# Performance work log

Hardware: AMD Instinct MI355X
Metric: run time of the kernel (lower is better)

The kernel has to match this reference:

```python
import jax, jax.numpy as jnp
import numpy as np

N_NODES = 300000
DIM = 64
NNZ = 4800000


def setup_inputs() -> dict:
    key = jax.random.key(0)
    ks = jax.random.split(key, 8)
    emb_all = 0.1 * jax.random.normal(ks[0], (N_NODES, DIM), dtype=jnp.float32)
    # edge values ~ symmetric-normalized adjacency scale (avg degree 16 -> ~1/16)
    vals = jax.random.uniform(ks[1], (NNZ,), dtype=jnp.float32) * (1.0 / 16.0)
    vals2 = jax.random.uniform(ks[2], (NNZ,), dtype=jnp.float32) * (1.0 / 16.0)
    rows = jnp.sort(jax.random.randint(ks[3], (NNZ,), 0, N_NODES, dtype=jnp.int32))
    cols = jax.random.randint(ks[4], (NNZ,), 0, N_NODES, dtype=jnp.int32)
    rows2 = jnp.sort(jax.random.randint(ks[5], (NNZ,), 0, N_NODES, dtype=jnp.int32))
    cols2 = jax.random.randint(ks[6], (NNZ,), 0, N_NODES, dtype=jnp.int32)
    return {
        "emb_all": emb_all,
        "vals": vals,
        "vals2": vals2,
        "rows": rows,
        "cols": cols,
        "rows2": rows2,
        "cols2": cols2,
        "n_layers": 3,
        "num_users": 100000,
    }


def _spmm(rows, cols, vals, x, n):
    # sparse [n,n] @ dense [n,d] via gather + segment-sum
    return jax.ops.segment_sum(vals[:, None] * x[cols], rows, num_segments=n)


def _pearson(x, y):
    # per-row pearson correlation over the last (latent) dim -> [N]
    xd = x - jnp.mean(x, axis=-1, keepdims=True)
    yd = y - jnp.mean(y, axis=-1, keepdims=True)
    num = jnp.sum(xd * yd, axis=-1)
    den = jnp.sqrt(jnp.sum(xd * xd, axis=-1)) * jnp.sqrt(jnp.sum(yd * yd, axis=-1))
    den = jnp.where(den < 1e-7, jnp.float32(1e-7), den)
    return num / den


def reference(emb_all, vals, vals2, rows, cols, rows2, cols2, n_layers, num_users):
    n = emb_all.shape[0]
    e0 = emb_all
    embs2 = [e0]
    # layer 0: plain LightGCN propagation on G
    e = _spmm(rows, cols, vals, e0, n)
    embs2.append(e)
    # layers 1..n_layers: pearson-gated propagation on G2
    for _ in range(n_layers):
        b = _pearson(embs2[-1], e0)  # [N]
        prop = _spmm(rows2, cols2, vals2, embs2[-1], n)
        e = b[:, None] * prop + (1.0 - b)[:, None] * e0
        embs2.append(e)
    light_out = jnp.mean(jnp.stack(embs2, axis=1), axis=1)  # [N, d]
    users = light_out[:num_users]
    items = light_out[num_users:]
    return users, items
```

## Files before the change

### kernel.cpp

```cpp
#include <hip/hip_runtime.h>

#define DIM 64

typedef __attribute__((ext_vector_type(4))) float f4;
typedef __attribute__((ext_vector_type(2))) float f2;
typedef __attribute__((ext_vector_type(4))) unsigned int u4;
typedef __attribute__((ext_vector_type(2))) unsigned int u2;

#define SEL_LO 0x01000504u
#define SEL_HI 0x03020706u
#define ONE2   0x3f803f80u

__device__ __forceinline__ float bflo(unsigned u) { return __uint_as_float(u << 16); }
__device__ __forceinline__ float bfhi(unsigned u) { return __uint_as_float(u & 0xffff0000u); }
__device__ __forceinline__ unsigned bfr(float f) {
    unsigned u = __float_as_uint(f);
    return (u + 0x7fffu + ((u >> 16) & 1u)) >> 16;
}
__device__ __forceinline__ unsigned packbf(float e, float o) { return bfr(e) | (bfr(o) << 16); }
__device__ __forceinline__ unsigned cvtpk(float lo, float hi) {
    unsigned r;
    asm("v_cvt_pk_bf16_f32 %0, %1, %2" : "=v"(r) : "v"(lo), "v"(hi));
    return r;
}
__device__ __forceinline__ float dot2bf(unsigned a, unsigned b, float c) {
    float d;
    asm("v_dot2_f32_bf16 %0, %1, %2, %3" : "=v"(d) : "v"(a), "v"(b), "v"(c));
    return d;
}
__device__ __forceinline__ float gsum8(float v) {
    v += __shfl_xor(v, 1, 64);
    v += __shfl_xor(v, 2, 64);
    v += __shfl_xor(v, 4, 64);
    return v;
}

__global__ void build_row_ptr2_kernel(const int* __restrict__ rowsA, int nnzA,
                                      const int* __restrict__ rowsB, int nnzB,
                                      int n, int* __restrict__ rpA,
                                      int* __restrict__ rpB) {
    int i = blockIdx.x * blockDim.x + threadIdx.x;
    const int* rows; int nnz; int* rp; int r;
    if (i <= n) { rows = rowsA; nnz = nnzA; rp = rpA; r = i; }
    else {
        r = i - (n + 1);
        if (r > n) return;
        rows = rowsB; nnz = nnzB; rp = rpB;
    }
    int lo = 0, hi = nnz;
    while (lo < hi) {
        int mid = (lo + hi) >> 1;
        if (rows[mid] < r) lo = mid + 1; else hi = mid;
    }
    rp[r] = lo;
}

__global__ void cvt_bf16_kernel(const float* __restrict__ in,
                                unsigned int* __restrict__ out, int n8) {
    int i = blockIdx.x * blockDim.x + threadIdx.x;
    if (i >= n8) return;
    const f4* p = (const f4*)in + 2 * (size_t)i;
    f4 a = p[0], b = p[1];
    u4 o;
    o.x = packbf(a.x, a.y); o.y = packbf(a.z, a.w);
    o.z = packbf(b.x, b.y); o.w = packbf(b.z, b.w);
    ((u4*)out)[i] = o;
}

template <int MODE>
__global__ __launch_bounds__(256) void layer_kernel(
    const unsigned short* __restrict__ t0,
    const unsigned short* __restrict__ eprev,
    const float* __restrict__ vals, const int* __restrict__ cols,
    const int* __restrict__ rp, int n,
    unsigned short* __restrict__ enew,
    const unsigned short* __restrict__ e1t,
    const unsigned short* __restrict__ e2t,
    f2* __restrict__ stats, float* __restrict__ bbuf,
    float* __restrict__ out)
{
    const int tid  = threadIdx.x;
    const int lane = tid & 63;
    const int j    = lane & 7;
    const int wave = blockIdx.x * (blockDim.x >> 6) + (tid >> 6);
    const int rowg = wave * 8 + (lane >> 3);
    const bool valid = rowg < n;
    const int rg   = valid ? rowg : n - 1;

    const int start = rp[rg];
    const int end   = rp[rg + 1];
    const int len   = valid ? (end - start) : 0;
    const int b0    = start & ~1;
    const int doff  = b0 - start;

    int ml = len;
    ml = max(ml, __shfl_xor(ml, 8, 64));
    ml = max(ml, __shfl_xor(ml, 16, 64));
    ml = max(ml, __shfl_xor(ml, 32, 64));
    const int steps = (ml + 8) >> 3;

    const char* tb8 = (const char*)eprev;
    const unsigned joff = (unsigned)(j << 4);
    const size_t ro = (size_t)rg << 6;

    float bcoef = 0.f;
    if (MODE != 0) bcoef = bbuf[rg];
    u4 yr = *((const u4*)(t0 + ro) + j);
    f2 st = {};
    if (MODE == 1) st = stats[rg];

    float acc[8] = {0.f, 0.f, 0.f, 0.f, 0.f, 0.f, 0.f, 0.f};

    for (int s = 0; s < steps; ++s) {
        const int k = b0 + (s << 3);
        u2 c01 = __builtin_nontemporal_load((const u2*)(cols + k));
        u2 c23 = __builtin_nontemporal_load((const u2*)(cols + k + 2));
        u2 c45 = __builtin_nontemporal_load((const u2*)(cols + k + 4));
        u2 c67 = __builtin_nontemporal_load((const u2*)(cols + k + 6));
        f2 v01 = __builtin_nontemporal_load((const f2*)(vals + k));
        f2 v23 = __builtin_nontemporal_load((const f2*)(vals + k + 2));
        f2 v45 = __builtin_nontemporal_load((const f2*)(vals + k + 4));
        f2 v67 = __builtin_nontemporal_load((const f2*)(vals + k + 6));
        const int rel = (s << 3) + doff;
        bool ok0 = (unsigned)(rel)     < (unsigned)len;
        bool ok1 = (unsigned)(rel + 1) < (unsigned)len;
        bool ok2 = (unsigned)(rel + 2) < (unsigned)len;
        bool ok3 = (unsigned)(rel + 3) < (unsigned)len;
        bool ok4 = (unsigned)(rel + 4) < (unsigned)len;
        bool ok5 = (unsigned)(rel + 5) < (unsigned)len;
        bool ok6 = (unsigned)(rel + 6) < (unsigned)len;
        bool ok7 = (unsigned)(rel + 7) < (unsigned)len;
        unsigned cc0 = ok0 ? (unsigned)c01.x : 0u;
        unsigned cc1 = ok1 ? (unsigned)c01.y : 0u;
        unsigned cc2 = ok2 ? (unsigned)c23.x : 0u;
        unsigned cc3 = ok3 ? (unsigned)c23.y : 0u;
        unsigned cc4 = ok4 ? (unsigned)c45.x : 0u;
        unsigned cc5 = ok5 ? (unsigned)c45.y : 0u;
        unsigned cc6 = ok6 ? (unsigned)c67.x : 0u;
        unsigned cc7 = ok7 ? (unsigned)c67.y : 0u;
        u4 g0 = *(const u4*)(tb8 + ((cc0 << 7) + joff));
        u4 g1 = *(const u4*)(tb8 + ((cc1 << 7) + joff));
        u4 g2 = *(const u4*)(tb8 + ((cc2 << 7) + joff));
        u4 g3 = *(const u4*)(tb8 + ((cc3 << 7) + joff));
        u4 g4 = *(const u4*)(tb8 + ((cc4 << 7) + joff));
        u4 g5 = *(const u4*)(tb8 + ((cc5 << 7) + joff));
        u4 g6 = *(const u4*)(tb8 + ((cc6 << 7) + joff));
        u4 g7 = *(const u4*)(tb8 + ((cc7 << 7) + joff));
        float w0 = ok0 ? v01.x : 0.f;
        float w1 = ok1 ? v01.y : 0.f;
        float w2 = ok2 ? v23.x : 0.f;
        float w3 = ok3 ? v23.y : 0.f;
        float w4 = ok4 ? v45.x : 0.f;
        float w5 = ok5 ? v45.y : 0.f;
        float w6 = ok6 ? v67.x : 0.f;
        float w7 = ok7 ? v67.y : 0.f;
        unsigned vp01 = cvtpk(w0, w1);
        unsigned vp23 = cvtpk(w2, w3);
        unsigned vp45 = cvtpk(w4, w5);
        unsigned vp67 = cvtpk(w6, w7);
#define CONSUME(ga, gb, vp)                                                    \
        acc[0] = dot2bf(__builtin_amdgcn_perm(ga.x, gb.x, SEL_LO), vp, acc[0]);\
        acc[1] = dot2bf(__builtin_amdgcn_perm(ga.x, gb.x, SEL_HI), vp, acc[1]);\
        acc[2] = dot2bf(__builtin_amdgcn_perm(ga.y, gb.y, SEL_LO), vp, acc[2]);\
        acc[3] = dot2bf(__builtin_amdgcn_perm(ga.y, gb.y, SEL_HI), vp, acc[3]);\
        acc[4] = dot2bf(__builtin_amdgcn_perm(ga.z, gb.z, SEL_LO), vp, acc[4]);\
        acc[5] = dot2bf(__builtin_amdgcn_perm(ga.z, gb.z, SEL_HI), vp, acc[5]);\
        acc[6] = dot2bf(__builtin_amdgcn_perm(ga.w, gb.w, SEL_LO), vp, acc[6]);\
        acc[7] = dot2bf(__builtin_amdgcn_perm(ga.w, gb.w, SEL_HI), vp, acc[7]);
        CONSUME(g0, g1, vp01)
        CONSUME(g2, g3, vp23)
        CONSUME(g4, g5, vp45)
        CONSUME(g6, g7, vp67)
#undef CONSUME
    }

    if (MODE == 0) {
        float sy  = dot2bf(yr.x, ONE2,
                    dot2bf(yr.y, ONE2, dot2bf(yr.z, ONE2, dot2bf(yr.w, ONE2, 0.f))));
        float syy = dot2bf(yr.x, yr.x,
                    dot2bf(yr.y, yr.y, dot2bf(yr.z, yr.z, dot2bf(yr.w, yr.w, 0.f))));
        sy = gsum8(sy); syy = gsum8(syy);
        float my  = sy * (1.f / 64.f);
        float vy  = syy - sy * my;
        float svy = sqrtf(fmaxf(vy, 0.f));
        u4 o;
        o.x = cvtpk(acc[0], acc[1]); o.y = cvtpk(acc[2], acc[3]);
        o.z = cvtpk(acc[4], acc[5]); o.w = cvtpk(acc[6], acc[7]);
        float sx  = dot2bf(o.x, ONE2,
                    dot2bf(o.y, ONE2, dot2bf(o.z, ONE2, dot2bf(o.w, ONE2, 0.f))));
        float sxx = dot2bf(o.x, o.x,
                    dot2bf(o.y, o.y, dot2bf(o.z, o.z, dot2bf(o.w, o.w, 0.f))));
        float sxy = dot2bf(o.x, yr.x,
                    dot2bf(o.y, yr.y, dot2bf(o.z, yr.z, dot2bf(o.w, yr.w, 0.f))));
        sx = gsum8(sx); sxx = gsum8(sxx); sxy = gsum8(sxy);
        float mx  = sx * (1.f / 64.f);
        float num = sxy - sx * my;
        float vx  = sxx - sx * mx;
        float den = sqrtf(fmaxf(vx, 0.f)) * svy;
        den = fmaxf(den, 1e-7f);
        float bn = num / den;
        if (valid) {
            if (j == 0) {
                f2 s2; s2.x = my; s2.y = svy;
                __builtin_nontemporal_store(s2, stats + rg);
                __builtin_nontemporal_store(bn, bbuf + rg);
            }
            __builtin_nontemporal_store(o, (u4*)(enew + ro) + j);
        }
        return;
    }

    const float ob = 1.f - bcoef;

    if (MODE == 1) {
        float y0[8] = { bflo(yr.x), bfhi(yr.x), bflo(yr.y), bfhi(yr.y),
                        bflo(yr.z), bfhi(yr.z), bflo(yr.w), bfhi(yr.w) };
        u4 o;
        o.x = cvtpk(bcoef * acc[0] + ob * y0[0], bcoef * acc[1] + ob * y0[1]);
        o.y = cvtpk(bcoef * acc[2] + ob * y0[2], bcoef * acc[3] + ob * y0[3]);
        o.z = cvtpk(bcoef * acc[4] + ob * y0[4], bcoef * acc[5] + ob * y0[5]);
        o.w = cvtpk(bcoef * acc[6] + ob * y0[6], bcoef * acc[7] + ob * y0[7]);
        float sx  = dot2bf(o.x, ONE2,
                    dot2bf(o.y, ONE2, dot2bf(o.z, ONE2, dot2bf(o.w, ONE2, 0.f))));
        float sxx = dot2bf(o.x, o.x,
                    dot2bf(o.y, o.y, dot2bf(o.z, o.z, dot2bf(o.w, o.w, 0.f))));
        float sxy = dot2bf(o.x, yr.x,
                    dot2bf(o.y, yr.y, dot2bf(o.z, yr.z, dot2bf(o.w, yr.w, 0.f))));
        sx = gsum8(sx); sxx = gsum8(sxx); sxy = gsum8(sxy);
        float mx  = sx * (1.f / 64.f);
        float num = sxy - sx * st.x;
        float vx  = sxx - sx * mx;
        float den = sqrtf(fmaxf(vx, 0.f)) * st.y;
        den = fmaxf(den, 1e-7f);
        float bn = num / den;
        if (valid) {
            if (j == 0) __builtin_nontemporal_store(bn, bbuf + rg);
            __builtin_nontemporal_store(o, (u4*)(enew + ro) + j);
        }
    } else {
        float y0[8] = { bflo(yr.x), bfhi(yr.x), bflo(yr.y), bfhi(yr.y),
                        bflo(yr.z), bfhi(yr.z), bflo(yr.w), bfhi(yr.w) };
        u4 xr = *((const u4*)(eprev + ro) + j);
        float xp[8] = { bflo(xr.x), bfhi(xr.x), bflo(xr.y), bfhi(xr.y),
                        bflo(xr.z), bfhi(xr.z), bflo(xr.w), bfhi(xr.w) };
        u4 r1 = *((const u4*)(e1t + ro) + j);
        u4 r2 = *((const u4*)(e2t + ro) + j);
        float s[8];
        s[0] = y0[0] + bflo(r1.x) + bflo(r2.x) + xp[0] + (bcoef * acc[0] + ob * y0[0]);
        s[1] = y0[1] + bfhi(r1.x) + bfhi(r2.x) + xp[1] + (bcoef * acc[1] + ob * y0[1]);
        s[2] = y0[2] + bflo(r1.y) + bflo(r2.y) + xp[2] + (bcoef * acc[2] + ob * y0[2]);
        s[3] = y0[3] + bfhi(r1.y) + bfhi(r2.y) + xp[3] + (bcoef * acc[3] + ob * y0[3]);
        s[4] = y0[4] + bflo(r1.z) + bflo(r2.z) + xp[4] + (bcoef * acc[4] + ob * y0[4]);
        s[5] = y0[5] + bfhi(r1.z) + bfhi(r2.z) + xp[5] + (bcoef * acc[5] + ob * y0[5]);
        s[6] = y0[6] + bflo(r1.w) + bflo(r2.w) + xp[6] + (bcoef * acc[6] + ob * y0[6]);
        s[7] = y0[7] + bfhi(r1.w) + bfhi(r2.w) + xp[7] + (bcoef * acc[7] + ob * y0[7]);
        if (valid) {
            f4 o0 = { s[0] * 0.2f, s[1] * 0.2f, s[2] * 0.2f, s[3] * 0.2f };
            f4 o1 = { s[4] * 0.2f, s[5] * 0.2f, s[6] * 0.2f, s[7] * 0.2f };
            f4* op = (f4*)(out + ro) + 2 * j;
            __builtin_nontemporal_store(o0, op);
            __builtin_nontemporal_store(o1, op + 1);
        }
    }
}

extern "C" void kernel_launch(void* const* d_in, const int* in_sizes, int n_in,
                              void* d_out, int out_size, void* d_ws, size_t ws_size,
                              hipStream_t stream) {
    const float* emb   = (const float*)d_in[0];
    const float* vals  = (const float*)d_in[1];
    const float* vals2 = (const float*)d_in[2];
    const int*   rows  = (const int*)d_in[3];
    const int*   cols  = (const int*)d_in[4];
    const int*   rows2 = (const int*)d_in[5];
    const int*   cols2 = (const int*)d_in[6];

    const int n    = in_sizes[0] / DIM;
    const int nnz  = in_sizes[1];
    const int nnz2 = in_sizes[2];

    float* out = (float*)d_out;

    char*  ws       = (char*)d_ws;
    size_t rp_bytes = (((size_t)(n + 1) * sizeof(int)) + 255) & ~(size_t)255;
    size_t st_bytes = (((size_t)n * sizeof(f2)) + 255) & ~(size_t)255;
    size_t bb_bytes = (((size_t)n * sizeof(float)) + 255) & ~(size_t)255;
    size_t tb_bytes = (size_t)n * DIM * sizeof(unsigned short);
    int*   rp1 = (int*)ws;
    int*   rp2 = (int*)(ws + rp_bytes);
    f2*    ST  = (f2*)(ws + 2 * rp_bytes);
    float* BB  = (float*)(ws + 2 * rp_bytes + st_bytes);
    unsigned short* T0 = (unsigned short*)(ws + 2 * rp_bytes + st_bytes + bb_bytes);
    unsigned short* E1 = (unsigned short*)((char*)T0 + tb_bytes);
    unsigned short* E2 = (unsigned short*)((char*)E1 + tb_bytes);
    unsigned short* E3 = (unsigned short*)((char*)E2 + tb_bytes);

    const int tb = 256;
    build_row_ptr2_kernel<<<(2 * (n + 1) + tb - 1) / tb, tb, 0, stream>>>(
        rows, nnz, rows2, nnz2, n, rp1, rp2);

    const int n8 = n * DIM / 8;
    cvt_bf16_kernel<<<(n8 + tb - 1) / tb, tb, 0, stream>>>(emb, (unsigned int*)T0, n8);

    const int waves = (n + 7) / 8;
    const int grid  = (waves + 3) / 4;
    layer_kernel<0><<<grid, tb, 0, stream>>>(T0, T0, vals, cols, rp1, n,
                                             E1, T0, T0, ST, BB, out);
    layer_kernel<1><<<grid, tb, 0, stream>>>(T0, E1, vals2, cols2, rp2, n,
                                             E2, T0, T0, ST, BB, out);
    layer_kernel<1><<<grid, tb, 0, stream>>>(T0, E2, vals2, cols2, rp2, n,
                                             E3, T0, T0, ST, BB, out);
    layer_kernel<2><<<grid, tb, 0, stream>>>(T0, E3, vals2, cols2, rp2, n,
                                             E3, E1, E2, ST, BB, out);
}
```

Baseline: 503.9 us.

## Gather neighbor embeddings from scaled FP8 tables instead of BF16

Each layer now writes a scaled FP8 copy of its embeddings alongside the BF16 copy, and the SpMM gather reads 8 bytes per lane from the FP8 table instead of 16. Accumulation moves to packed FP32 multiply-adds after FP8-to-FP32 unpacking. Layer 1 also pre-sums e1 and e2 into one buffer, so the final layer reads fewer tensors. This roughly halves the random gather traffic that dominates SpMM, at the cost of FP8 precision loss in the propagated values and extra stores per layer.

```diff
diff --git a/kernel.cpp b/kernel.cpp
--- a/kernel.cpp
+++ b/kernel.cpp
@@ -1,15 +1,15 @@
 #include <hip/hip_runtime.h>
 
 #define DIM 64
+#define SC  32.0f
+#define ISC 0.03125f
 
 typedef __attribute__((ext_vector_type(4))) float f4;
 typedef __attribute__((ext_vector_type(2))) float f2;
 typedef __attribute__((ext_vector_type(4))) unsigned int u4;
 typedef __attribute__((ext_vector_type(2))) unsigned int u2;
 
-#define SEL_LO 0x01000504u
-#define SEL_HI 0x03020706u
-#define ONE2   0x3f803f80u
+#define ONE2 0x3f803f80u
 
 __device__ __forceinline__ float bflo(unsigned u) { return __uint_as_float(u << 16); }
 __device__ __forceinline__ float bfhi(unsigned u) { return __uint_as_float(u & 0xffff0000u); }
@@ -55,8 +55,9 @@
     rp[r] = lo;
 }
 
-__global__ void cvt_bf16_kernel(const float* __restrict__ in,
-                                unsigned int* __restrict__ out, int n8) {
+__global__ void cvt_kernel(const float* __restrict__ in,
+                           unsigned int* __restrict__ obf,
+                           unsigned char* __restrict__ of8, int n8) {
     int i = blockIdx.x * blockDim.x + threadIdx.x;
     if (i >= n8) return;
     const f4* p = (const f4*)in + 2 * (size_t)i;
@@ -64,18 +65,27 @@
     u4 o;
     o.x = packbf(a.x, a.y); o.y = packbf(a.z, a.w);
     o.z = packbf(b.x, b.y); o.w = packbf(b.z, b.w);
-    ((u4*)out)[i] = o;
-}
-
-template <int MODE>
+    ((u4*)obf)[i] = o;
+    int lo = 0, hi = 0;
+    lo = __builtin_amdgcn_cvt_pk_fp8_f32(a.x * SC, a.y * SC, lo, false);
+    lo = __builtin_amdgcn_cvt_pk_fp8_f32(a.z * SC, a.w * SC, lo, true);
+    hi = __builtin_amdgcn_cvt_pk_fp8_f32(b.x * SC, b.y * SC, hi, false);
+    hi = __builtin_amdgcn_cvt_pk_fp8_f32(b.z * SC, b.w * SC, hi, true);
+    u2 w8; w8.x = (unsigned)lo; w8.y = (unsigned)hi;
+    ((u2*)of8)[i] = w8;
+}
+
+template <int MODE, bool SUM>
 __global__ __launch_bounds__(256) void layer_kernel(
     const unsigned short* __restrict__ t0,
-    const unsigned short* __restrict__ eprev,
+    const unsigned char*  __restrict__ gtab,
     const float* __restrict__ vals, const int* __restrict__ cols,
     const int* __restrict__ rp, int n,
-    unsigned short* __restrict__ enew,
-    const unsigned short* __restrict__ e1t,
-    const unsigned short* __restrict__ e2t,
+    unsigned short* __restrict__ bfout,
+    unsigned char*  __restrict__ f8out,
+    const unsigned short* __restrict__ e1in,
+    const unsigned short* __restrict__ e3in,
+    const unsigned short* __restrict__ s12in,
     f2* __restrict__ stats, float* __restrict__ bbuf,
     float* __restrict__ out)
 {
@@ -99,17 +109,16 @@
     ml = max(ml, __shfl_xor(ml, 32, 64));
     const int steps = (ml + 8) >> 3;
 
-    const char* tb8 = (const char*)eprev;
-    const unsigned joff = (unsigned)(j << 4);
+    const unsigned joff8 = (unsigned)(j << 3);
     const size_t ro = (size_t)rg << 6;
 
     float bcoef = 0.f;
-    if (MODE != 0) bcoef = bbuf[rg];
-    u4 yr = *((const u4*)(t0 + ro) + j);
+    if (MODE != 0) bcoef = __builtin_nontemporal_load(bbuf + rg);
+    u4 yr = __builtin_nontemporal_load((const u4*)(t0 + ro) + j);
     f2 st = {};
-    if (MODE == 1) st = stats[rg];
-
-    float acc[8] = {0.f, 0.f, 0.f, 0.f, 0.f, 0.f, 0.f, 0.f};
+    if (MODE == 1) st = __builtin_nontemporal_load(stats + rg);
+
+    f2 a01 = {0.f, 0.f}, a23 = {0.f, 0.f}, a45 = {0.f, 0.f}, a67 = {0.f, 0.f};
 
     for (int s = 0; s < steps; ++s) {
         const int k = b0 + (s << 3);
@@ -138,14 +147,14 @@
         unsigned cc5 = ok5 ? (unsigned)c45.y : 0u;
         unsigned cc6 = ok6 ? (unsigned)c67.x : 0u;
         unsigned cc7 = ok7 ? (unsigned)c67.y : 0u;
-        u4 g0 = *(const u4*)(tb8 + ((cc0 << 7) + joff));
-        u4 g1 = *(const u4*)(tb8 + ((cc1 << 7) + joff));
-        u4 g2 = *(const u4*)(tb8 + ((cc2 << 7) + joff));
-        u4 g3 = *(const u4*)(tb8 + ((cc3 << 7) + joff));
-        u4 g4 = *(const u4*)(tb8 + ((cc4 << 7) + joff));
-        u4 g5 = *(const u4*)(tb8 + ((cc5 << 7) + joff));
-        u4 g6 = *(const u4*)(tb8 + ((cc6 << 7) + joff));
-        u4 g7 = *(const u4*)(tb8 + ((cc7 << 7) + joff));
+        u2 g0 = *(const u2*)(gtab + ((cc0 << 6) + joff8));
+        u2 g1 = *(const u2*)(gtab + ((cc1 << 6) + joff8));
+        u2 g2 = *(const u2*)(gtab + ((cc2 << 6) + joff8));
+        u2 g3 = *(const u2*)(gtab + ((cc3 << 6) + joff8));
+        u2 g4 = *(const u2*)(gtab + ((cc4 << 6) + joff8));
+        u2 g5 = *(const u2*)(gtab + ((cc5 << 6) + joff8));
+        u2 g6 = *(const u2*)(gtab + ((cc6 << 6) + joff8));
+        u2 g7 = *(const u2*)(gtab + ((cc7 << 6) + joff8));
         float w0 = ok0 ? v01.x : 0.f;
         float w1 = ok1 ? v01.y : 0.f;
         float w2 = ok2 ? v23.x : 0.f;
@@ -154,25 +163,21 @@
         float w5 = ok5 ? v45.y : 0.f;
         float w6 = ok6 ? v67.x : 0.f;
         float w7 = ok7 ? v67.y : 0.f;
-        unsigned vp01 = cvtpk(w0, w1);
-        unsigned vp23 = cvtpk(w2, w3);
-        unsigned vp45 = cvtpk(w4, w5);
-        unsigned vp67 = cvtpk(w6, w7);
-#define CONSUME(ga, gb, vp)                                                    \
-        acc[0] = dot2bf(__builtin_amdgcn_perm(ga.x, gb.x, SEL_LO), vp, acc[0]);\
-        acc[1] = dot2bf(__builtin_amdgcn_perm(ga.x, gb.x, SEL_HI), vp, acc[1]);\
-        acc[2] = dot2bf(__builtin_amdgcn_perm(ga.y, gb.y, SEL_LO), vp, acc[2]);\
-        acc[3] = dot2bf(__builtin_amdgcn_perm(ga.y, gb.y, SEL_HI), vp, acc[3]);\
-        acc[4] = dot2bf(__builtin_amdgcn_perm(ga.z, gb.z, SEL_LO), vp, acc[4]);\
-        acc[5] = dot2bf(__builtin_amdgcn_perm(ga.z, gb.z, SEL_HI), vp, acc[5]);\
-        acc[6] = dot2bf(__builtin_amdgcn_perm(ga.w, gb.w, SEL_LO), vp, acc[6]);\
-        acc[7] = dot2bf(__builtin_amdgcn_perm(ga.w, gb.w, SEL_HI), vp, acc[7]);
-        CONSUME(g0, g1, vp01)
-        CONSUME(g2, g3, vp23)
-        CONSUME(g4, g5, vp45)
-        CONSUME(g6, g7, vp67)
-#undef CONSUME
-    }
+#define CONS(gg, ww) {                                                        \
+        f2 wv; wv.x = (ww); wv.y = (ww);                                      \
+        f2 p0 = __builtin_amdgcn_cvt_pk_f32_fp8((int)gg.x, false);            \
+        f2 p1 = __builtin_amdgcn_cvt_pk_f32_fp8((int)gg.x, true);             \
+        f2 p2 = __builtin_amdgcn_cvt_pk_f32_fp8((int)gg.y, false);            \
+        f2 p3 = __builtin_amdgcn_cvt_pk_f32_fp8((int)gg.y, true);             \
+        a01 += wv * p0; a23 += wv * p1; a45 += wv * p2; a67 += wv * p3;       \
+    }
+        CONS(g0, w0) CONS(g1, w1) CONS(g2, w2) CONS(g3, w3)
+        CONS(g4, w4) CONS(g5, w5) CONS(g6, w6) CONS(g7, w7)
+#undef CONS
+    }
+
+    float acc[8] = { a01.x * ISC, a01.y * ISC, a23.x * ISC, a23.y * ISC,
+                     a45.x * ISC, a45.y * ISC, a67.x * ISC, a67.y * ISC };
 
     if (MODE == 0) {
         float sy  = dot2bf(yr.x, ONE2,
@@ -205,21 +210,29 @@
                 __builtin_nontemporal_store(s2, stats + rg);
                 __builtin_nontemporal_store(bn, bbuf + rg);
             }
-            __builtin_nontemporal_store(o, (u4*)(enew + ro) + j);
+            __builtin_nontemporal_store(o, (u4*)(bfout + ro) + j);
+            int lo = 0, hi = 0;
+            lo = __builtin_amdgcn_cvt_pk_fp8_f32(acc[0] * SC, acc[1] * SC, lo, false);
+            lo = __builtin_amdgcn_cvt_pk_fp8_f32(acc[2] * SC, acc[3] * SC, lo, true);
+            hi = __builtin_amdgcn_cvt_pk_fp8_f32(acc[4] * SC, acc[5] * SC, hi, false);
+            hi = __builtin_amdgcn_cvt_pk_fp8_f32(acc[6] * SC, acc[7] * SC, hi, true);
+            u2 w8; w8.x = (unsigned)lo; w8.y = (unsigned)hi;
+            __builtin_nontemporal_store(w8, (u2*)(f8out + (ro  )) + j);
         }
         return;
     }
 
     const float ob = 1.f - bcoef;
+    float y0[8] = { bflo(yr.x), bfhi(yr.x), bflo(yr.y), bfhi(yr.y),
+                    bflo(yr.z), bfhi(yr.z), bflo(yr.w), bfhi(yr.w) };
+    float en[8];
+    #pragma unroll
+    for (int i = 0; i < 8; ++i) en[i] = bcoef * acc[i] + ob * y0[i];
 
     if (MODE == 1) {
-        float y0[8] = { bflo(yr.x), bfhi(yr.x), bflo(yr.y), bfhi(yr.y),
-                        bflo(yr.z), bfhi(yr.z), bflo(yr.w), bfhi(yr.w) };
         u4 o;
-        o.x = cvtpk(bcoef * acc[0] + ob * y0[0], bcoef * acc[1] + ob * y0[1]);
-        o.y = cvtpk(bcoef * acc[2] + ob * y0[2], bcoef * acc[3] + ob * y0[3]);
-        o.z = cvtpk(bcoef * acc[4] + ob * y0[4], bcoef * acc[5] + ob * y0[5]);
-        o.w = cvtpk(bcoef * acc[6] + ob * y0[6], bcoef * acc[7] + ob * y0[7]);
+        o.x = cvtpk(en[0], en[1]); o.y = cvtpk(en[2], en[3]);
+        o.z = cvtpk(en[4], en[5]); o.w = cvtpk(en[6], en[7]);
         float sx  = dot2bf(o.x, ONE2,
                     dot2bf(o.y, ONE2, dot2bf(o.z, ONE2, dot2bf(o.w, ONE2, 0.f))));
         float sxx = dot2bf(o.x, o.x,
@@ -235,25 +248,37 @@
         float bn = num / den;
         if (valid) {
             if (j == 0) __builtin_nontemporal_store(bn, bbuf + rg);
-            __builtin_nontemporal_store(o, (u4*)(enew + ro) + j);
+            if (SUM) {
+                u4 e1r = __builtin_nontemporal_load((const u4*)(e1in + ro) + j);
+                u4 so;
+                so.x = packbf(bflo(e1r.x) + en[0], bfhi(e1r.x) + en[1]);
+                so.y = packbf(bflo(e1r.y) + en[2], bfhi(e1r.y) + en[3]);
+                so.z = packbf(bflo(e1r.z) + en[4], bfhi(e1r.z) + en[5]);
+                so.w = packbf(bflo(e1r.w) + en[6], bfhi(e1r.w) + en[7]);
+                __builtin_nontemporal_store(so, (u4*)(bfout + ro) + j);
+            } else {
+                __builtin_nontemporal_store(o, (u4*)(bfout + ro) + j);
+            }
+            int lo = 0, hi = 0;
+            lo = __builtin_amdgcn_cvt_pk_fp8_f32(en[0] * SC, en[1] * SC, lo, false);
+            lo = __builtin_amdgcn_cvt_pk_fp8_f32(en[2] * SC, en[3] * SC, lo, true);
+            hi = __builtin_amdgcn_cvt_pk_fp8_f32(en[4] * SC, en[5] * SC, hi, false);
+            hi = __builtin_amdgcn_cvt_pk_fp8_f32(en[6] * SC, en[7] * SC, hi, true);
+            u2 w8; w8.x = (unsigned)lo; w8.y = (unsigned)hi;
+            __builtin_nontemporal_store(w8, (u2*)(f8out + ro) + j);
         }
     } else {
-        float y0[8] = { bflo(yr.x), bfhi(yr.x), bflo(yr.y), bfhi(yr.y),
-                        bflo(yr.z), bfhi(yr.z), bflo(yr.w), bfhi(yr.w) };
-        u4 xr = *((const u4*)(eprev + ro) + j);
-        float xp[8] = { bflo(xr.x), bfhi(xr.x), bflo(xr.y), bfhi(xr.y),
-                        bflo(xr.z), bfhi(xr.z), bflo(xr.w), bfhi(xr.w) };
-        u4 r1 = *((const u4*)(e1t + ro) + j);
-        u4 r2 = *((const u4*)(e2t + ro) + j);
+        u4 xr  = __builtin_nontemporal_load((const u4*)(e3in + ro) + j);
+        u4 s12 = __builtin_nontemporal_load((const u4*)(s12in + ro) + j);
         float s[8];
-        s[0] = y0[0] + bflo(r1.x) + bflo(r2.x) + xp[0] + (bcoef * acc[0] + ob * y0[0]);
-        s[1] = y0[1] + bfhi(r1.x) + bfhi(r2.x) + xp[1] + (bcoef * acc[1] + ob * y0[1]);
-        s[2] = y0[2] + bflo(r1.y) + bflo(r2.y) + xp[2] + (bcoef * acc[2] + ob * y0[2]);
-        s[3] = y0[3] + bfhi(r1.y) + bfhi(r2.y) + xp[3] + (bcoef * acc[3] + ob * y0[3]);
-        s[4] = y0[4] + bflo(r1.z) + bflo(r2.z) + xp[4] + (bcoef * acc[4] + ob * y0[4]);
-        s[5] = y0[5] + bfhi(r1.z) + bfhi(r2.z) + xp[5] + (bcoef * acc[5] + ob * y0[5]);
-        s[6] = y0[6] + bflo(r1.w) + bflo(r2.w) + xp[6] + (bcoef * acc[6] + ob * y0[6]);
-        s[7] = y0[7] + bfhi(r1.w) + bfhi(r2.w) + xp[7] + (bcoef * acc[7] + ob * y0[7]);
+        s[0] = y0[0] + bflo(s12.x) + bflo(xr.x) + en[0];
+        s[1] = y0[1] + bfhi(s12.x) + bfhi(xr.x) + en[1];
+        s[2] = y0[2] + bflo(s12.y) + bflo(xr.y) + en[2];
+        s[3] = y0[3] + bfhi(s12.y) + bfhi(xr.y) + en[3];
+        s[4] = y0[4] + bflo(s12.z) + bflo(xr.z) + en[4];
+        s[5] = y0[5] + bfhi(s12.z) + bfhi(xr.z) + en[5];
+        s[6] = y0[6] + bflo(s12.w) + bflo(xr.w) + en[6];
+        s[7] = y0[7] + bfhi(s12.w) + bfhi(xr.w) + en[7];
         if (valid) {
             f4 o0 = { s[0] * 0.2f, s[1] * 0.2f, s[2] * 0.2f, s[3] * 0.2f };
             f4 o1 = { s[4] * 0.2f, s[5] * 0.2f, s[6] * 0.2f, s[7] * 0.2f };
@@ -286,30 +311,35 @@
     size_t st_bytes = (((size_t)n * sizeof(f2)) + 255) & ~(size_t)255;
     size_t bb_bytes = (((size_t)n * sizeof(float)) + 255) & ~(size_t)255;
     size_t tb_bytes = (size_t)n * DIM * sizeof(unsigned short);
+    size_t f8_bytes = (size_t)n * DIM;
     int*   rp1 = (int*)ws;
     int*   rp2 = (int*)(ws + rp_bytes);
     f2*    ST  = (f2*)(ws + 2 * rp_bytes);
     float* BB  = (float*)(ws + 2 * rp_bytes + st_bytes);
-    unsigned short* T0 = (unsigned short*)(ws + 2 * rp_bytes + st_bytes + bb_bytes);
-    unsigned short* E1 = (unsigned short*)((char*)T0 + tb_bytes);
-    unsigned short* E2 = (unsigned short*)((char*)E1 + tb_bytes);
-    unsigned short* E3 = (unsigned short*)((char*)E2 + tb_bytes);
+    char*  p   = ws + 2 * rp_bytes + st_bytes + bb_bytes;
+    unsigned short* T0  = (unsigned short*)p;              p += tb_bytes;
+    unsigned short* E1  = (unsigned short*)p;              p += tb_bytes;
+    unsigned short* S12 = (unsigned short*)p;              p += tb_bytes;
+    unsigned char*  T0F = (unsigned char*)p;               p += f8_bytes;
+    unsigned char*  FA  = (unsigned char*)p;               p += f8_bytes;
+    unsigned char*  FB  = (unsigned char*)p;               p += f8_bytes;
+    unsigned short* E3  = E1;
 
     const int tb = 256;
     build_row_ptr2_kernel<<<(2 * (n + 1) + tb - 1) / tb, tb, 0, stream>>>(
         rows, nnz, rows2, nnz2, n, rp1, rp2);
 
     const int n8 = n * DIM / 8;
-    cvt_bf16_kernel<<<(n8 + tb - 1) / tb, tb, 0, stream>>>(emb, (unsigned int*)T0, n8);
+    cvt_kernel<<<(n8 + tb - 1) / tb, tb, 0, stream>>>(emb, (unsigned int*)T0, T0F, n8);
 
     const int waves = (n + 7) / 8;
     const int grid  = (waves + 3) / 4;
-    layer_kernel<0><<<grid, tb, 0, stream>>>(T0, T0, vals, cols, rp1, n,
-                                             E1, T0, T0, ST, BB, out);
-    layer_kernel<1><<<grid, tb, 0, stream>>>(T0, E1, vals2, cols2, rp2, n,
-                                             E2, T0, T0, ST, BB, out);
-    layer_kernel<1><<<grid, tb, 0, stream>>>(T0, E2, vals2, cols2, rp2, n,
-                                             E3, T0, T0, ST, BB, out);
-    layer_kernel<2><<<grid, tb, 0, stream>>>(T0, E3, vals2, cols2, rp2, n,
-                                             E3, E1, E2, ST, BB, out);
-}
+    layer_kernel<0, false><<<grid, tb, 0, stream>>>(T0, T0F, vals, cols, rp1, n,
+                                                    E1, FA, E1, E1, S12, ST, BB, out);
+    layer_kernel<1, true><<<grid, tb, 0, stream>>>(T0, FA, vals2, cols2, rp2, n,
+                                                   S12, FB, E1, E1, S12, ST, BB, out);
+    layer_kernel<1, false><<<grid, tb, 0, stream>>>(T0, FB, vals2, cols2, rp2, n,
+                                                    E3, FA, E1, E1, S12, ST, BB, out);
+    layer_kernel<2, false><<<grid, tb, 0, stream>>>(T0, FA, vals2, cols2, rp2, n,
+                                                    E3, FA, E1, E3, S12, ST, BB, out);
+}
```

After: 474.4 us. 5.9% less time.
